# Kernel tuning notes

Hardware: AMD Instinct MI355X
Metric: run time of the kernel (lower is better)

## Reference

```python
import jax, jax.numpy as jnp
import numpy as np

DIM_IN = 1024
DIM_OUT = 1024
BATCH = 4
SEQ = 2048


def setup_inputs() -> dict:
    key = jax.random.key(0)
    kx, kq, kk, kv = jax.random.split(key, 4)
    scale = 1.0 / np.sqrt(DIM_IN)
    x = jax.random.normal(kx, (BATCH, SEQ, DIM_IN), dtype=jnp.float32)
    # Weights stored as [dim_in, dim_out] (transpose of torch Linear's [out, in]);
    # y = x @ W is equivalent math to torch's x @ W_t.T
    Wq = jax.random.normal(kq, (DIM_IN, DIM_OUT), dtype=jnp.float32) * scale
    Wk = jax.random.normal(kk, (DIM_IN, DIM_OUT), dtype=jnp.float32) * scale
    Wv = jax.random.normal(kv, (DIM_IN, DIM_OUT), dtype=jnp.float32) * scale
    return {"x": x, "Wq": Wq, "Wk": Wk, "Wv": Wv}


def reference(x, Wq, Wk, Wv):
    # x: [b, s, d_in]; single-head causal self-attention (dropout=0 -> identity)
    q = jnp.einsum("bsd,de->bse", x, Wq)
    k = jnp.einsum("bsd,de->bse", x, Wk)
    v = jnp.einsum("bsd,de->bse", x, Wv)
    dim_k = k.shape[-1]
    scores = jnp.einsum("bqe,bke->bqk", q, k) / jnp.sqrt(jnp.float32(dim_k))
    s = x.shape[1]
    causal = jnp.tril(jnp.ones((s, s), dtype=bool))  # True = keep
    scores = jnp.where(causal[None, :, :], scores, -jnp.inf)
    weights = jax.nn.softmax(scores, axis=-1)
    context = jnp.einsum("bqk,bke->bqe", weights, v)
    return context
```

## Files before the change

### kernel.cpp

```cpp
#include <hip/hip_runtime.h>
#include <cstdint>
#include <cstddef>

typedef unsigned short u16;
typedef __bf16 bf16x8 __attribute__((ext_vector_type(8)));
typedef float f32x4 __attribute__((ext_vector_type(4)));

__device__ inline u16 f2b(float f) {
    uint32_t u = __builtin_bit_cast(uint32_t, f);
    u += 0x7FFFu + ((u >> 16) & 1u);
    return (u16)(u >> 16);
}

__device__ inline void gl2lds16(const u16* g, u16* l) {
    __builtin_amdgcn_global_load_lds(
        (const __attribute__((address_space(1))) void*)g,
        (__attribute__((address_space(3))) void*)l, 16, 0, 0);
}

__global__ void prep_kernel(const float* __restrict__ x, u16* __restrict__ xb,
                            const float* __restrict__ Wq,
                            const float* __restrict__ Wk,
                            const float* __restrict__ Wv,
                            u16* __restrict__ QKWT, u16* __restrict__ WvT,
                            float* __restrict__ l) {
    __shared__ u16 t[32][33];
    const int bid = blockIdx.x;
    if (bid < 8192) {
        size_t i = ((size_t)bid * 256 + threadIdx.x) * 4;
        float4 v = *(const float4*)(x + i);
        uint2 pack;
        pack.x = (uint32_t)f2b(v.x) | ((uint32_t)f2b(v.y) << 16);
        pack.y = (uint32_t)f2b(v.z) | ((uint32_t)f2b(v.w) << 16);
        *(uint2*)(xb + i) = pack;
        return;
    }
    if (bid >= 11264) {
        size_t i = ((size_t)(bid - 11264) * 256 + threadIdx.x) * 4;
        *(float4*)(l + i) = make_float4(0.f, 0.f, 0.f, 0.f);
        return;
    }
    const int tb = bid - 8192;
    const int z = tb >> 10;
    const int rem = tb & 1023;
    const int by = (rem >> 5) * 32;
    const int bx = (rem & 31) * 32;
    const float* W = (z == 0) ? Wq : ((z == 1) ? Wk : Wv);
    u16* dst = (z == 0) ? QKWT : ((z == 1) ? QKWT + 1024 * 1024 : WvT);
    const float scale = (z == 0) ? 0.03125f : 1.0f;
    const int tx = threadIdx.x & 31, ty = threadIdx.x >> 5;
    #pragma unroll
    for (int r = 0; r < 32; r += 8)
        t[ty + r][tx] = f2b(W[(size_t)(by + ty + r) * 1024 + bx + tx] * scale);
    __syncthreads();
    #pragma unroll
    for (int r = 0; r < 32; r += 8)
        dst[(size_t)(bx + ty + r) * 1024 + (by + tx)] = t[tx][ty + r];
}

template<int EPI>
__device__ __forceinline__ void gemm_body(
    u16* __restrict__ smem,
    const u16* __restrict__ A, int lda,
    const u16* __restrict__ B, int ldb,
    char* __restrict__ Cb, int ldc,
    int m0, int n0, int Kloc, float* __restrict__ lrow) {
    constexpr int BK = 32;
    const int tid = threadIdx.x;
    const int lane = tid & 63, wave = tid >> 6;
    const int wm = wave >> 1, wn = wave & 1;
    const int fl = lane & 15, fh = lane >> 4;

    const int q0 = wave * 2;
    const int srow = lane >> 2, skoff = (lane & 3) * 8;
    const u16* ApL0 = A + (size_t)(m0 + q0 * 16 + srow) * lda + skoff;
    const u16* ApL1 = ApL0 + (size_t)16 * lda;
    const u16* BpL0 = B + (size_t)(n0 + q0 * 16 + srow) * ldb + skoff;
    const u16* BpL1 = BpL0 + (size_t)16 * ldb;

    u16* const Ab[2] = { smem, smem + 4096 };
    u16* const Bb[2] = { smem + 8192, smem + 12288 };

    auto issue = [&](int buf, int k0) {
        gl2lds16(ApL0 + k0, Ab[buf] + q0 * 512);
        gl2lds16(ApL1 + k0, Ab[buf] + q0 * 512 + 512);
        gl2lds16(BpL0 + k0, Bb[buf] + q0 * 512);
        gl2lds16(BpL1 + k0, Bb[buf] + q0 * 512 + 512);
    };

    const f32x4 vzero = {0.f, 0.f, 0.f, 0.f};
    f32x4 acc[4][4];
    #pragma unroll
    for (int i = 0; i < 4; ++i)
        #pragma unroll
        for (int j = 0; j < 4; ++j) acc[i][j] = vzero;

    issue(0, 0);
    int buf = 0;
    for (int k0 = 0; k0 < Kloc; k0 += BK, buf ^= 1) {
        __syncthreads();
        if (k0 + BK < Kloc) issue(buf ^ 1, k0 + BK);
        bf16x8 af[4], bfr[4];
        #pragma unroll
        for (int t = 0; t < 4; ++t) {
            af[t]  = *(const bf16x8*)&Ab[buf][(wm * 64 + t * 16 + fl) * BK + fh * 8];
            bfr[t] = *(const bf16x8*)&Bb[buf][(wn * 64 + t * 16 + fl) * BK + fh * 8];
        }
        #pragma unroll
        for (int mt = 0; mt < 4; ++mt)
            #pragma unroll
            for (int nt = 0; nt < 4; ++nt)
                acc[mt][nt] = __builtin_amdgcn_mfma_f32_16x16x32_bf16(
                    af[mt], bfr[nt], acc[mt][nt], 0, 0, 0);
    }

    if (EPI == 0) {
        u16* Cp = (u16*)Cb;
        #pragma unroll
        for (int mt = 0; mt < 4; ++mt)
            #pragma unroll
            for (int nt = 0; nt < 4; ++nt)
                #pragma unroll
                for (int r = 0; r < 4; ++r) {
                    int row = m0 + wm * 64 + mt * 16 + fh * 4 + r;
                    int col = n0 + wn * 64 + nt * 16 + fl;
                    Cp[(size_t)row * ldc + col] = f2b(acc[mt][nt][r]);
                }
    } else if (EPI == 2) {
        u16* Cp = (u16*)Cb;
        #pragma unroll
        for (int mt = 0; mt < 4; ++mt)
            #pragma unroll
            for (int r = 0; r < 4; ++r) {
                int row = m0 + wm * 64 + mt * 16 + fh * 4 + r;
                float part = 0.f;
                #pragma unroll
                for (int nt = 0; nt < 4; ++nt) {
                    int col = n0 + wn * 64 + nt * 16 + fl;
                    float p = (col <= row) ? __expf(acc[mt][nt][r]) : 0.f;
                    part += p;
                    Cp[(size_t)row * ldc + col] = f2b(p);
                }
                #pragma unroll
                for (int off = 1; off < 16; off <<= 1)
                    part += __shfl_xor(part, off, 64);
                if (fl == 0) atomicAdd(lrow + row, part);
            }
    } else {
        float* Cp = (float*)Cb;
        #pragma unroll
        for (int mt = 0; mt < 4; ++mt)
            #pragma unroll
            for (int r = 0; r < 4; ++r) {
                int row = m0 + wm * 64 + mt * 16 + fh * 4 + r;
                float inv = 1.0f / lrow[row];
                #pragma unroll
                for (int nt = 0; nt < 4; ++nt) {
                    int col = n0 + wn * 64 + nt * 16 + fl;
                    Cp[(size_t)row * ldc + col] = acc[mt][nt][r] * inv;
                }
            }
    }
}

__global__ __launch_bounds__(256)
void projqk_kernel(const u16* __restrict__ xb, const u16* __restrict__ QKWT,
                   u16* __restrict__ QK) {
    __shared__ __align__(16) u16 smem[16384];
    const int jt = blockIdx.x & 15, it = blockIdx.x >> 4;
    gemm_body<0>(smem, xb, 1024, QKWT, 1024, (char*)QK, 2048,
                 it * 128, jt * 128, 1024, nullptr);
}

__global__ __launch_bounds__(256)
void mid_kernel(const u16* __restrict__ QK, u16* __restrict__ P,
                float* __restrict__ l,
                const u16* __restrict__ WvT, const u16* __restrict__ xb,
                u16* __restrict__ Vt) {
    __shared__ __align__(16) u16 smem[16384];
    const int bid = blockIdx.x;
    if (bid < 544) {
        const int z = bid / 136, t = bid - z * 136;
        int it = (int)((sqrtf(8.0f * t + 1.0f) - 1.0f) * 0.5f);
        while ((it + 1) * (it + 2) / 2 <= t) ++it;
        while (it * (it + 1) / 2 > t) --it;
        const int jt = t - it * (it + 1) / 2;
        const u16* Qz = QK + (size_t)z * 2048 * 2048;
        const u16* Kz = Qz + 1024;
        u16* Pz = P + (size_t)z * 2048 * 2048;
        gemm_body<2>(smem, Qz, 2048, Kz, 2048, (char*)Pz, 2048,
                     it * 128, jt * 128, 1024, l + (size_t)z * 2048);
    } else {
        const int b = bid - 544;
        const int jt = b & 63, it = b >> 6;
        gemm_body<0>(smem, WvT, 1024, xb, 1024, (char*)Vt, 8192,
                     it * 128, jt * 128, 1024, nullptr);
    }
}

__global__ __launch_bounds__(256)
void out_kernel(const u16* __restrict__ P, const u16* __restrict__ Vt,
                float* __restrict__ out, float* __restrict__ l) {
    __shared__ __align__(16) u16 smem[16384];
    const int jt = blockIdx.x & 7, z = blockIdx.x >> 3;
    const int it = 15 - (int)blockIdx.y;
    gemm_body<3>(smem, P + (size_t)z * 2048 * 2048, 2048,
                 Vt + (size_t)z * 2048, 8192,
                 (char*)(out + (size_t)z * 2048 * 1024), 1024,
                 it * 128, jt * 128, (it + 1) * 128, l + (size_t)z * 2048);
}

extern "C" void kernel_launch(void* const* d_in, const int* in_sizes, int n_in,
                              void* d_out, int out_size, void* d_ws, size_t ws_size,
                              hipStream_t stream) {
    (void)in_sizes; (void)n_in; (void)out_size; (void)ws_size;
    const float* x  = (const float*)d_in[0];
    const float* Wq = (const float*)d_in[1];
    const float* Wk = (const float*)d_in[2];
    const float* Wv = (const float*)d_in[3];
    float* out = (float*)d_out;

    const size_t MB = 1u << 20;
    char* ws = (char*)d_ws;
    u16* xb   = (u16*)(ws);
    u16* QKWT = (u16*)(ws + 16 * MB);
    u16* WvT  = (u16*)(ws + 20 * MB);
    u16* QK   = (u16*)(ws + 22 * MB);
    u16* Vt   = (u16*)(ws + 54 * MB);
    u16* P    = (u16*)(ws + 70 * MB);
    float* l  = (float*)(ws + 102 * MB);

    prep_kernel<<<8192 + 3072 + 8, 256, 0, stream>>>(x, xb, Wq, Wk, Wv, QKWT, WvT, l);
    projqk_kernel<<<1024, 256, 0, stream>>>(xb, QKWT, QK);
    mid_kernel<<<1056, 256, 0, stream>>>(QK, P, l, WvT, xb, Vt);
    out_kernel<<<dim3(32, 16), 256, 0, stream>>>(P, Vt, out, l);
}
```

Measured before the change: 258.0 us.

## Fuse all stages into one persistent kernel with atomic job queues and grid barriers

Replaces the four separate launches (prep, QK projection, scores, output) with a single persistent kernel of 768 blocks. Blocks pull work from per-phase atomic counters and separate phases with software grid barriers. The V projection now runs alongside the QK projection rather than with the score stage. This removes launch gaps and tail idling between kernels, but adds atomic and barrier overhead and relies on all 768 blocks being co-resident to avoid deadlock.

```diff
diff --git a/kernel.cpp b/kernel.cpp
--- a/kernel.cpp
+++ b/kernel.cpp
@@ -3,8 +3,11 @@
 #include <cstddef>
 
 typedef unsigned short u16;
+typedef unsigned int u32;
 typedef __bf16 bf16x8 __attribute__((ext_vector_type(8)));
 typedef float f32x4 __attribute__((ext_vector_type(4)));
+
+#define NBLK 768
 
 __device__ inline u16 f2b(float f) {
     uint32_t u = __builtin_bit_cast(uint32_t, f);
@@ -16,46 +19,6 @@
     __builtin_amdgcn_global_load_lds(
         (const __attribute__((address_space(1))) void*)g,
         (__attribute__((address_space(3))) void*)l, 16, 0, 0);
-}
-
-__global__ void prep_kernel(const float* __restrict__ x, u16* __restrict__ xb,
-                            const float* __restrict__ Wq,
-                            const float* __restrict__ Wk,
-                            const float* __restrict__ Wv,
-                            u16* __restrict__ QKWT, u16* __restrict__ WvT,
-                            float* __restrict__ l) {
-    __shared__ u16 t[32][33];
-    const int bid = blockIdx.x;
-    if (bid < 8192) {
-        size_t i = ((size_t)bid * 256 + threadIdx.x) * 4;
-        float4 v = *(const float4*)(x + i);
-        uint2 pack;
-        pack.x = (uint32_t)f2b(v.x) | ((uint32_t)f2b(v.y) << 16);
-        pack.y = (uint32_t)f2b(v.z) | ((uint32_t)f2b(v.w) << 16);
-        *(uint2*)(xb + i) = pack;
-        return;
-    }
-    if (bid >= 11264) {
-        size_t i = ((size_t)(bid - 11264) * 256 + threadIdx.x) * 4;
-        *(float4*)(l + i) = make_float4(0.f, 0.f, 0.f, 0.f);
-        return;
-    }
-    const int tb = bid - 8192;
-    const int z = tb >> 10;
-    const int rem = tb & 1023;
-    const int by = (rem >> 5) * 32;
-    const int bx = (rem & 31) * 32;
-    const float* W = (z == 0) ? Wq : ((z == 1) ? Wk : Wv);
-    u16* dst = (z == 0) ? QKWT : ((z == 1) ? QKWT + 1024 * 1024 : WvT);
-    const float scale = (z == 0) ? 0.03125f : 1.0f;
-    const int tx = threadIdx.x & 31, ty = threadIdx.x >> 5;
-    #pragma unroll
-    for (int r = 0; r < 32; r += 8)
-        t[ty + r][tx] = f2b(W[(size_t)(by + ty + r) * 1024 + bx + tx] * scale);
-    __syncthreads();
-    #pragma unroll
-    for (int r = 0; r < 32; r += 8)
-        dst[(size_t)(bx + ty + r) * 1024 + (by + tx)] = t[tx][ty + r];
 }
 
 template<int EPI>
@@ -163,51 +126,118 @@
     }
 }
 
-__global__ __launch_bounds__(256)
-void projqk_kernel(const u16* __restrict__ xb, const u16* __restrict__ QKWT,
-                   u16* __restrict__ QK) {
+__global__ __launch_bounds__(256, 3)
+void mega_kernel(const float* __restrict__ x,
+                 const float* __restrict__ Wq, const float* __restrict__ Wk,
+                 const float* __restrict__ Wv, float* __restrict__ out,
+                 u16* __restrict__ xb, u16* __restrict__ QKWT,
+                 u16* __restrict__ WvT, u16* __restrict__ QK,
+                 u16* __restrict__ Vt, u16* __restrict__ P,
+                 float* __restrict__ l, u32* ctrl) {
     __shared__ __align__(16) u16 smem[16384];
-    const int jt = blockIdx.x & 15, it = blockIdx.x >> 4;
-    gemm_body<0>(smem, xb, 1024, QKWT, 1024, (char*)QK, 2048,
-                 it * 128, jt * 128, 1024, nullptr);
-}
-
-__global__ __launch_bounds__(256)
-void mid_kernel(const u16* __restrict__ QK, u16* __restrict__ P,
-                float* __restrict__ l,
-                const u16* __restrict__ WvT, const u16* __restrict__ xb,
-                u16* __restrict__ Vt) {
-    __shared__ __align__(16) u16 smem[16384];
-    const int bid = blockIdx.x;
-    if (bid < 544) {
-        const int z = bid / 136, t = bid - z * 136;
-        int it = (int)((sqrtf(8.0f * t + 1.0f) - 1.0f) * 0.5f);
-        while ((it + 1) * (it + 2) / 2 <= t) ++it;
-        while (it * (it + 1) / 2 > t) --it;
-        const int jt = t - it * (it + 1) / 2;
+    __shared__ int jobLds;
+    const int tid = threadIdx.x;
+
+    auto nextjob = [&](int phase) -> int {
+        if (tid == 0) jobLds = (int)atomicAdd(&ctrl[phase], 1u);
+        __syncthreads();
+        int j = jobLds;
+        __syncthreads();
+        return j;
+    };
+    auto gbar = [&](int idx) {
+        __syncthreads();
+        __threadfence();
+        if (tid == 0) {
+            atomicAdd(&ctrl[idx], 1u);
+            while (atomicAdd(&ctrl[idx], 0u) < NBLK) __builtin_amdgcn_s_sleep(8);
+        }
+        __syncthreads();
+        __threadfence();
+    };
+
+    for (;;) {
+        int j = nextjob(0);
+        if (j >= 5122) break;
+        if (j < 2048) {
+            size_t base = (size_t)j * 4096;
+            #pragma unroll
+            for (int r = 0; r < 4; ++r) {
+                size_t i = base + (size_t)(r * 256 + tid) * 4;
+                float4 v = *(const float4*)(x + i);
+                uint2 pack;
+                pack.x = (u32)f2b(v.x) | ((u32)f2b(v.y) << 16);
+                pack.y = (u32)f2b(v.z) | ((u32)f2b(v.w) << 16);
+                *(uint2*)(xb + i) = pack;
+            }
+        } else if (j < 5120) {
+            const int tb = j - 2048;
+            const int z = tb >> 10, rem = tb & 1023;
+            const int by = (rem >> 5) * 32, bx = (rem & 31) * 32;
+            const float* W = (z == 0) ? Wq : ((z == 1) ? Wk : Wv);
+            u16* dst = (z == 0) ? QKWT : ((z == 1) ? QKWT + 1024 * 1024 : WvT);
+            const float scale = (z == 0) ? 0.03125f : 1.0f;
+            u16 (*t)[33] = (u16(*)[33])smem;
+            const int tx = tid & 31, ty = tid >> 5;
+            #pragma unroll
+            for (int r = 0; r < 32; r += 8)
+                t[ty + r][tx] = f2b(W[(size_t)(by + ty + r) * 1024 + bx + tx] * scale);
+            __syncthreads();
+            #pragma unroll
+            for (int r = 0; r < 32; r += 8)
+                dst[(size_t)(bx + ty + r) * 1024 + (by + tx)] = t[tx][ty + r];
+        } else {
+            size_t base = (size_t)(j - 5120) * 4096;
+            #pragma unroll
+            for (int r = 0; r < 4; ++r)
+                *(float4*)(l + base + (size_t)(r * 256 + tid) * 4) =
+                    make_float4(0.f, 0.f, 0.f, 0.f);
+        }
+    }
+    gbar(4);
+
+    for (;;) {
+        int j = nextjob(1);
+        if (j >= 1536) break;
+        if (j < 1024) {
+            int it = j >> 4, jt = j & 15;
+            gemm_body<0>(smem, xb, 1024, QKWT, 1024, (char*)QK, 2048,
+                         it * 128, jt * 128, 1024, nullptr);
+        } else {
+            int b = j - 1024, it = b >> 6, jt = b & 63;
+            gemm_body<0>(smem, WvT, 1024, xb, 1024, (char*)Vt, 8192,
+                         it * 128, jt * 128, 1024, nullptr);
+        }
+    }
+    gbar(5);
+
+    for (;;) {
+        int j = nextjob(2);
+        if (j >= 544) break;
+        const int z = j & 3;
+        int t = j >> 2, it = 15, jt = 0;
+        for (int i = 15; i >= 0; --i) {
+            int n = i + 1;
+            if (t < n) { it = i; jt = t; break; }
+            t -= n;
+        }
         const u16* Qz = QK + (size_t)z * 2048 * 2048;
-        const u16* Kz = Qz + 1024;
-        u16* Pz = P + (size_t)z * 2048 * 2048;
-        gemm_body<2>(smem, Qz, 2048, Kz, 2048, (char*)Pz, 2048,
+        gemm_body<2>(smem, Qz, 2048, Qz + 1024, 2048,
+                     (char*)(P + (size_t)z * 2048 * 2048), 2048,
                      it * 128, jt * 128, 1024, l + (size_t)z * 2048);
-    } else {
-        const int b = bid - 544;
-        const int jt = b & 63, it = b >> 6;
-        gemm_body<0>(smem, WvT, 1024, xb, 1024, (char*)Vt, 8192,
-                     it * 128, jt * 128, 1024, nullptr);
-    }
-}
-
-__global__ __launch_bounds__(256)
-void out_kernel(const u16* __restrict__ P, const u16* __restrict__ Vt,
-                float* __restrict__ out, float* __restrict__ l) {
-    __shared__ __align__(16) u16 smem[16384];
-    const int jt = blockIdx.x & 7, z = blockIdx.x >> 3;
-    const int it = 15 - (int)blockIdx.y;
-    gemm_body<3>(smem, P + (size_t)z * 2048 * 2048, 2048,
-                 Vt + (size_t)z * 2048, 8192,
-                 (char*)(out + (size_t)z * 2048 * 1024), 1024,
-                 it * 128, jt * 128, (it + 1) * 128, l + (size_t)z * 2048);
+    }
+    gbar(6);
+
+    for (;;) {
+        int j = nextjob(3);
+        if (j >= 512) break;
+        const int z = j & 3, r = j >> 2;
+        const int it = 15 - (r >> 3), jt = r & 7;
+        gemm_body<3>(smem, P + (size_t)z * 2048 * 2048, 2048,
+                     Vt + (size_t)z * 2048, 8192,
+                     (char*)(out + (size_t)z * 2048 * 1024), 1024,
+                     it * 128, jt * 128, (it + 1) * 128, l + (size_t)z * 2048);
+    }
 }
 
 extern "C" void kernel_launch(void* const* d_in, const int* in_sizes, int n_in,
@@ -229,9 +259,9 @@
     u16* Vt   = (u16*)(ws + 54 * MB);
     u16* P    = (u16*)(ws + 70 * MB);
     float* l  = (float*)(ws + 102 * MB);
-
-    prep_kernel<<<8192 + 3072 + 8, 256, 0, stream>>>(x, xb, Wq, Wk, Wv, QKWT, WvT, l);
-    projqk_kernel<<<1024, 256, 0, stream>>>(xb, QKWT, QK);
-    mid_kernel<<<1056, 256, 0, stream>>>(QK, P, l, WvT, xb, Vt);
-    out_kernel<<<dim3(32, 16), 256, 0, stream>>>(P, Vt, out, l);
-}
+    u32* ctrl = (u32*)(ws + 103 * MB);
+
+    hipMemsetAsync(ctrl, 0, 64, stream);
+    mega_kernel<<<NBLK, 256, 0, stream>>>(x, Wq, Wk, Wv, out,
+                                          xb, QKWT, WvT, QK, Vt, P, l, ctrl);
+}
```

New measurement: 943.5 us. +265.7%, slower.
